# Performance work log

Measured on AMD Instinct MI355X. Metric: run time of the kernel, lower is better.

The kernel has to match this reference:

```python
import jax, jax.numpy as jnp
import numpy as np

FEAT_STRIDE = 16
PRE_NMS_TOP_N = 6000
POST_NMS_TOP_N = 300
NMS_THRESH = 0.7
MIN_SIZE = 16.0
SCALES = np.array([8.0, 16.0, 32.0])
RATIOS = np.array([0.5, 1.0, 2.0])


def _whctrs(a):
    w = a[2] - a[0] + 1.0
    h = a[3] - a[1] + 1.0
    return w, h, a[0] + 0.5 * (w - 1.0), a[1] + 0.5 * (h - 1.0)


def _mkanchors(ws, hs, xc, yc):
    ws = np.asarray(ws).reshape(-1, 1)
    hs = np.asarray(hs).reshape(-1, 1)
    return np.hstack([xc - 0.5 * (ws - 1.0), yc - 0.5 * (hs - 1.0),
                      xc + 0.5 * (ws - 1.0), yc + 0.5 * (hs - 1.0)])


def generate_anchors(base_size, ratios, scales):
    base = np.array([1.0, 1.0, base_size, base_size]) - 1.0
    w, h, xc, yc = _whctrs(base)
    size = w * h
    ws = np.round(np.sqrt(size / ratios))
    hs = np.round(ws * ratios)
    ratio_anchors = _mkanchors(ws, hs, xc, yc)
    out = []
    for i in range(ratio_anchors.shape[0]):
        w, h, xc, yc = _whctrs(ratio_anchors[i])
        out.append(_mkanchors(w * scales, h * scales, xc, yc))
    return np.vstack(out)


def _nms(boxes, scores, thresh, max_out):
    # greedy NMS, boxes [N,4], scores [N] (-inf = invalid). Returns idx [max_out], valid [max_out]
    N = boxes.shape[0]
    x1, y1, x2, y2 = boxes[:, 0], boxes[:, 1], boxes[:, 2], boxes[:, 3]
    areas = (x2 - x1 + 1.0) * (y2 - y1 + 1.0)
    ar = jnp.arange(N)

    def step(s, _):
        i = jnp.argmax(s)
        valid = s[i] > -jnp.inf
        b = boxes[i]
        xx1 = jnp.maximum(b[0], x1)
        yy1 = jnp.maximum(b[1], y1)
        xx2 = jnp.minimum(b[2], x2)
        yy2 = jnp.minimum(b[3], y2)
        inter = jnp.maximum(0.0, xx2 - xx1 + 1.0) * jnp.maximum(0.0, yy2 - yy1 + 1.0)
        iou = inter / (areas[i] + areas - inter)
        sup = (iou > thresh) | (ar == i)
        return jnp.where(sup, -jnp.inf, s), (i, valid)

    _, (idx, valid) = jax.lax.scan(step, scores, None, length=max_out)
    return idx, valid


def setup_inputs() -> dict:
    key = jax.random.key(0)
    k1, k2 = jax.random.split(key)
    B, A, Hf, Wf = 16, 9, 160, 160
    scores_map = jax.random.uniform(k1, (B, 2 * A, Hf, Wf), dtype=jnp.float32)
    bbox_deltas = jax.random.normal(k2, (B, 4 * A, Hf, Wf), dtype=jnp.float32) * 0.2
    im_info = jnp.tile(jnp.array([[Hf * FEAT_STRIDE, Wf * FEAT_STRIDE, 1.0]], jnp.float32), (B, 1))
    return {"scores_map": scores_map, "bbox_deltas": bbox_deltas, "im_info": im_info}


def reference(scores_map, bbox_deltas, im_info):
    anchors0 = jnp.asarray(generate_anchors(16, RATIOS, SCALES), jnp.float32)  # [A,4]
    A = anchors0.shape[0]
    B, _, Hf, Wf = scores_map.shape
    # fg scores: [B, A, H, W] -> [B, H*W*A]
    scores = scores_map[:, A:].transpose(0, 2, 3, 1).reshape(B, -1)
    deltas = bbox_deltas.transpose(0, 2, 3, 1).reshape(B, -1, 4)  # [B, H*W*A, 4]
    sx = (jnp.arange(Wf) * FEAT_STRIDE).astype(jnp.float32)
    sy = (jnp.arange(Hf) * FEAT_STRIDE).astype(jnp.float32)
    SX, SY = jnp.meshgrid(sx, sy)  # [H, W]
    shifts = jnp.stack([SX.ravel(), SY.ravel(), SX.ravel(), SY.ravel()], axis=1)  # [K,4]
    all_anchors = (shifts[:, None, :] + anchors0[None, :, :]).reshape(-1, 4)  # [K*A, 4]

    aw = all_anchors[:, 2] - all_anchors[:, 0] + 1.0
    ah = all_anchors[:, 3] - all_anchors[:, 1] + 1.0
    acx = all_anchors[:, 0] + 0.5 * aw
    acy = all_anchors[:, 1] + 0.5 * ah

    def single(s, d, info):
        # bbox_transform_inv
        pcx = d[:, 0] * aw + acx
        pcy = d[:, 1] * ah + acy
        pw = jnp.exp(d[:, 2]) * aw
        ph = jnp.exp(d[:, 3]) * ah
        x1 = jnp.clip(pcx - 0.5 * pw, 0.0, info[1] - 1.0)
        y1 = jnp.clip(pcy - 0.5 * ph, 0.0, info[0] - 1.0)
        x2 = jnp.clip(pcx + 0.5 * pw, 0.0, info[1] - 1.0)
        y2 = jnp.clip(pcy + 0.5 * ph, 0.0, info[0] - 1.0)
        boxes = jnp.stack([x1, y1, x2, y2], axis=1)
        ms = MIN_SIZE * info[2]
        keep = ((x2 - x1 + 1.0) >= ms) & ((y2 - y1 + 1.0) >= ms)
        s = jnp.where(keep, s, -jnp.inf)
        top_s, top_i = jax.lax.top_k(s, PRE_NMS_TOP_N)
        top_b = boxes[top_i]
        idx, valid = _nms(top_b, top_s, NMS_THRESH, POST_NMS_TOP_N)
        return jnp.where(valid[:, None], top_b[idx], 0.0)  # [POST, 4]

    out_boxes = jax.vmap(single)(scores, deltas, im_info)  # [B, POST, 4]
    batch_col = jnp.broadcast_to(
        jnp.arange(B, dtype=out_boxes.dtype)[:, None, None], (B, POST_NMS_TOP_N, 1))
    return jnp.concatenate([batch_col, out_boxes], axis=2)  # [B, POST, 5]
```

## Files before the change

### kernel.cpp

```cpp
#include <hip/hip_runtime.h>
#include <cstdint>
#include <cstddef>

typedef unsigned int u32;
typedef unsigned long long u64;

#define NBATCH 16
#define NA 9
#define HF 160
#define WF 160
#define HWC (HF*WF)
#define NPB (NA*HWC)
#define PRE_N 6000
#define POST_N 300
#define SEL_CAP 8192
#define NBIN 2048
#define UNI_BINS 2048
#define NMS_W 16

__constant__ float c_AW[9] = {184.f,368.f,736.f,128.f,256.f,512.f,88.f,176.f,352.f};
__constant__ float c_AH[9] = {96.f,192.f,384.f,128.f,256.f,512.f,176.f,352.f,704.f};

__device__ __forceinline__ void box_core(
    float d0, float d1, float d2, float d3, int a, int x, int y,
    float imH, float imW, float ms,
    float& x1, float& y1, float& x2, float& y2, bool& keep)
{
  float aw = c_AW[a], ah = c_AH[a];
  float acx = (float)x * 16.0f + 8.0f;
  float acy = (float)y * 16.0f + 8.0f;
  float pcx = d0 * aw + acx;
  float pcy = d1 * ah + acy;
  float pw  = expf(d2) * aw;
  float ph  = expf(d3) * ah;
  x1 = fminf(fmaxf(pcx - 0.5f * pw, 0.0f), imW - 1.0f);
  y1 = fminf(fmaxf(pcy - 0.5f * ph, 0.0f), imH - 1.0f);
  x2 = fminf(fmaxf(pcx + 0.5f * pw, 0.0f), imW - 1.0f);
  y2 = fminf(fmaxf(pcy + 0.5f * ph, 0.0f), imH - 1.0f);
  keep = ((x2 - x1 + 1.0f) >= ms) && ((y2 - y1 + 1.0f) >= ms);
}

__device__ __forceinline__ void box_from_deltas(
    const float* __restrict__ bd, int b, int a, int pos,
    float imH, float imW, float ms,
    float& x1, float& y1, float& x2, float& y2, bool& keep)
{
  int y = pos / WF;
  int x = pos - y * WF;
  size_t base = ((size_t)(b * 4 * NA) + 4 * a) * HWC + (size_t)pos;
  float d0 = bd[base];
  float d1 = bd[base + HWC];
  float d2 = bd[base + 2 * HWC];
  float d3 = bd[base + 3 * HWC];
  box_core(d0, d1, d2, d3, a, x, y, imH, imW, ms, x1, y1, x2, y2, keep);
}

__device__ __forceinline__ u32 desc_enc(float s) {
  u32 su = __float_as_uint(s);
  u32 asc = (su & 0x80000000u) ? ~su : (su | 0x80000000u);
  return ~asc;
}

__device__ __forceinline__ bool iou_gt(float inter, float uni) {
  float ss = fmaf(0.7f, uni, -inter);
  if (fabsf(ss) <= uni * 1e-6f) return (inter / uni > 0.7f);
  return ss < 0.0f;
}

__global__ void __launch_bounds__(256) k_scores_hist(
    const float* __restrict__ sm, const float* __restrict__ bd,
    const float* __restrict__ info, u32* __restrict__ keys, u32* __restrict__ hist) {
  __shared__ u32 lh[UNI_BINS];
  int img   = blockIdx.x / 45;
  int rem   = blockIdx.x - img * 45;
  int a     = rem / 5;
  int chunk = rem - a * 5;
  int tid = threadIdx.x;
  for (int i = tid; i < UNI_BINS; i += 256) lh[i] = 0;
  __syncthreads();
  float imH = info[img*3+0], imW = info[img*3+1], ms = 16.0f * info[img*3+2];
  const float* sp = sm + ((size_t)(img * 2 * NA) + NA + a) * HWC;
  const float* dp = bd + ((size_t)(img * 4 * NA) + 4 * a) * HWC;
  u32* kp = keys + (size_t)img * NPB + (size_t)a * HWC;
  for (int j = 0; j < 5; j++) {
    int pos0 = (chunk * 1280 + j * 256 + tid) * 4;
    float4 s4  = *(const float4*)&sp[pos0];
    float4 q0  = *(const float4*)&dp[pos0];
    float4 q1  = *(const float4*)&dp[HWC + pos0];
    float4 q2  = *(const float4*)&dp[2*HWC + pos0];
    float4 q3  = *(const float4*)&dp[3*HWC + pos0];
    float sv[4] = {s4.x, s4.y, s4.z, s4.w};
    float v0[4] = {q0.x, q0.y, q0.z, q0.w};
    float v1[4] = {q1.x, q1.y, q1.z, q1.w};
    float v2[4] = {q2.x, q2.y, q2.z, q2.w};
    float v3[4] = {q3.x, q3.y, q3.z, q3.w};
    u32 kq[4];
    #pragma unroll
    for (int e = 0; e < 4; e++) {
      int pos = pos0 + e;
      int y = pos / WF;
      int x = pos - y * WF;
      float x1, y1, x2, y2; bool keep;
      box_core(v0[e], v1[e], v2[e], v3[e], a, x, y, imH, imW, ms, x1, y1, x2, y2, keep);
      float s = sv[e];
      if (!keep) s = __uint_as_float(0xFF800000u);
      kq[e] = desc_enc(s);
      int q = (int)floorf(s * (float)UNI_BINS);
      q = q < 0 ? 0 : (q > UNI_BINS - 1 ? UNI_BINS - 1 : q);
      atomicAdd(&lh[(UNI_BINS - 1) - q], 1u);
    }
    *(uint4*)&kp[pos0] = make_uint4(kq[0], kq[1], kq[2], kq[3]);
  }
  __syncthreads();
  u32* gh = hist + img * UNI_BINS;
  for (int i = tid; i < UNI_BINS; i += 256) { u32 v = lh[i]; if (v) atomicAdd(&gh[i], v); }
}

__global__ void __launch_bounds__(256) k_select(
    const u32* __restrict__ keys, const u32* __restrict__ hist, u64* __restrict__ thresh_arr) {
  int img = blockIdx.x, tid = threadIdx.x;
  __shared__ u32 sc[256];
  __shared__ u32 lh[NBIN];
  __shared__ u64 sh_thresh;
  __shared__ int sh_state;
  __shared__ u64 sh_prefix;
  __shared__ u32 sh_kth;
  const u32* gh = hist + img * UNI_BINS;
  u32 loc[8]; u32 tot = 0;
  for (int j = 0; j < 8; j++) { loc[j] = gh[tid * 8 + j]; tot += loc[j]; }
  if (tid == 0) { sh_state = 0; sh_prefix = 0; sh_kth = PRE_N; }
  sc[tid] = tot;
  __syncthreads();
  for (int off = 1; off < 256; off <<= 1) {
    u32 v = sc[tid]; u32 a = (tid >= off) ? sc[tid - off] : 0u;
    __syncthreads(); sc[tid] = v + a; __syncthreads();
  }
  u32 incl = sc[tid], excl = incl - tot;
  if (PRE_N > excl && PRE_N <= incl) {
    u32 run = excl;
    for (int j = 0; j < 8; j++) {
      run += loc[j];
      if (run >= PRE_N) {
        int b = tid * 8 + j;
        if (b < UNI_BINS - 1 && run <= SEL_CAP) {
          float sb = (float)(UNI_BINS - 1 - b) * (1.0f / (float)UNI_BINS);
          sh_thresh = ((u64)desc_enc(sb) << 32) | 0xFFFFFFFFull;
          sh_state = 1;
        }
        break;
      }
    }
  }
  __syncthreads();
  if (!sh_state) {
    const u32* kp = keys + (size_t)img * NPB;
    const int shifts[6] = {53, 42, 31, 20, 9, 0};
    const int widths[6] = {11, 11, 11, 11, 11, 9};
    for (int p = 0; p < 6; p++) {
      if (sh_state) break;
      for (int i = tid; i < NBIN; i += 256) lh[i] = 0;
      __syncthreads();
      u64 prefix = sh_prefix; u32 kth = sh_kth;
      int shift = shifts[p], width = widths[p];
      u32 nb = 1u << width;
      int hs = shift + width;
      for (int i = tid; i < NPB; i += 256) {
        int a = i / HWC;
        int pos = i - a * HWC;
        u64 key = ((u64)kp[i] << 32) | (u64)(u32)(pos * NA + a);
        bool m = (p == 0) || ((key >> hs) == prefix);
        if (m) atomicAdd(&lh[(u32)(key >> shift) & (nb - 1u)], 1u);
      }
      __syncthreads();
      u32 l2[8]; u32 t2 = 0;
      for (int j = 0; j < 8; j++) {
        u32 b = (u32)(tid * 8 + j);
        u32 v = (b < nb) ? lh[b] : 0u;
        l2[j] = v; t2 += v;
      }
      sc[tid] = t2; __syncthreads();
      for (int off = 1; off < 256; off <<= 1) {
        u32 v = sc[tid]; u32 a = (tid >= off) ? sc[tid - off] : 0u;
        __syncthreads(); sc[tid] = v + a; __syncthreads();
      }
      u32 incl2 = sc[tid], excl2 = incl2 - t2;
      if (kth > excl2 && kth <= incl2) {
        u32 run = excl2;
        for (int j = 0; j < 8; j++) {
          run += l2[j];
          if (run >= kth) {
            u32 bin = (u32)(tid * 8 + j);
            u32 below = run - l2[j];
            u32 cnt = l2[j];
            u32 knew = kth - below;
            u64 pfull = (prefix << width) | (u64)bin;
            u32 M = (u32)PRE_N - knew + cnt;
            if (M <= SEL_CAP) {
              u64 lowmask = (shift > 0) ? ((1ULL << shift) - 1ULL) : 0ULL;
              sh_thresh = (pfull << shift) | lowmask;
              sh_state = 1;
            } else {
              sh_prefix = pfull; sh_kth = knew;
            }
            break;
          }
        }
      }
      __syncthreads();
    }
  }
  if (tid == 0) thresh_arr[img] = sh_thresh;
}

__global__ void __launch_bounds__(256) k_compact(
    const u32* __restrict__ keys, const u64* __restrict__ thresh,
    u32* __restrict__ selcnt, u64* __restrict__ sel,
    const float* __restrict__ bd, const float* __restrict__ info,
    float4* __restrict__ boxsel) {
  int img = blockIdx.y;
  int tid = threadIdx.x;
  u64 T = thresh[img];
  int t0 = blockIdx.x * 3840;
  const u32* kp = keys + (size_t)img * NPB + t0;
  u64 fk[15];
  u32 mycnt = 0;
  #pragma unroll
  for (int j = 0; j < 15; j++) {
    int t = t0 + j * 256 + tid;
    u32 d = kp[j * 256 + tid];
    int a = t / HWC;
    int pos = t - a * HWC;
    u64 key = ((u64)d << 32) | (u64)(u32)(pos * NA + a);
    fk[j] = key;
    if (key <= T) mycnt++;
  }
  __shared__ u32 sc[256];
  __shared__ u32 sbase;
  sc[tid] = mycnt;
  __syncthreads();
  for (int off = 1; off < 256; off <<= 1) {
    u32 v = sc[tid];
    u32 add = (tid >= off) ? sc[tid - off] : 0u;
    __syncthreads();
    sc[tid] = v + add;
    __syncthreads();
  }
  if (tid == 255 && sc[255] > 0) sbase = atomicAdd(&selcnt[img], sc[255]);
  __syncthreads();
  if (mycnt == 0) return;
  u32 myoff = sbase + sc[tid] - mycnt;
  u64* sp = sel + (size_t)img * SEL_CAP;
  float4* bp = boxsel + (size_t)img * SEL_CAP;
  float imH = info[img*3+0], imW = info[img*3+1], ms = 16.0f * info[img*3+2];
  u32 c = 0;
  #pragma unroll
  for (int j = 0; j < 15; j++) {
    u64 key = fk[j];
    if (key <= T) {
      u32 p = myoff + c;
      if (p < SEL_CAP) {
        u32 desc = (u32)(key >> 32);
        u32 idx = (u32)key;
        sp[p] = ((u64)desc << 31) | ((u64)idx << 13) | (u64)p;
        int a = (int)(idx % NA);
        int pos = (int)(idx / NA);
        float x1, y1, x2, y2; bool keep;
        box_from_deltas(bd, img, a, pos, imH, imW, ms, x1, y1, x2, y2, keep);
        bp[p] = make_float4(x1, y1, x2, y2);
      }
      c++;
    }
  }
}

__global__ void __launch_bounds__(256) k_sort1(u64* __restrict__ sel, const u32* __restrict__ selcnt) {
  __shared__ u64 s[1024];
  int img = blockIdx.y, c = blockIdx.x, tid = threadIdx.x;
  u32 cnt = selcnt[img]; if (cnt > SEL_CAP) cnt = SEL_CAP;
  u64* sp = sel + (size_t)img * SEL_CAP + (size_t)c * 1024;
  int gbase = c * 1024;
  for (int i = tid; i < 1024; i += 256) s[i] = ((u32)(gbase + i) < cnt) ? sp[i] : ~0ULL;
  __syncthreads();
  for (int k = 2; k <= 1024; k <<= 1) {
    for (int j = k >> 1; j > 0; j >>= 1) {
      for (int i = tid; i < 1024; i += 256) {
        int p = i ^ j;
        if (p > i) {
          u64 a = s[i], b = s[p];
          bool up = ((i & k) == 0);
          if (up ? (a > b) : (a < b)) { s[i] = b; s[p] = a; }
        }
      }
      __syncthreads();
    }
  }
  for (int i = tid; i < 1024; i += 256) sp[i] = s[i];
}

__global__ void __launch_bounds__(1024) k_sort2(
    const u64* __restrict__ sel, const float4* __restrict__ boxsel,
    float4* __restrict__ boxes, u32* __restrict__ nvalid) {
  __shared__ u64 s[SEL_CAP];
  __shared__ int sh_nv;
  int img = blockIdx.x;
  int tid = threadIdx.x;
  const u64* sp = sel + (size_t)img * SEL_CAP;
  if (tid == 0) sh_nv = PRE_N;
  for (int i = tid; i < SEL_CAP; i += 1024) s[i] = sp[i];
  __syncthreads();
  int d0 = tid * 8;
  for (int L = 1024; L < SEL_CAP; L <<= 1) {
    int pairBase = d0 & ~(2 * L - 1);
    int d = d0 - pairBase;
    const u64* A = s + pairBase;
    const u64* B = s + pairBase + L;
    int lo = d - L; if (lo < 0) lo = 0;
    int hi = (d < L) ? d : L;
    while (lo < hi) {
      int mid = (lo + hi) >> 1;
      if (A[mid] <= B[d - 1 - mid]) lo = mid + 1; else hi = mid;
    }
    int ia = lo, ib = d - lo;
    u64 o[8];
    #pragma unroll
    for (int k = 0; k < 8; k++) {
      bool ta = (ib >= L) || (ia < L && A[ia] <= B[ib]);
      o[k] = ta ? A[ia++] : B[ib++];
    }
    __syncthreads();
    #pragma unroll
    for (int k = 0; k < 8; k++) s[d0 + k] = o[k];
    __syncthreads();
  }
  const float4* bp = boxsel + (size_t)img * SEL_CAP;
  for (int r = tid; r < PRE_N; r += 1024) {
    u64 key = s[r];
    u32 desc = (u32)(key >> 31);
    bool valid = desc < 0xFF800000u;
    if (!valid) atomicMin(&sh_nv, r);
    float4 bx = valid ? bp[key & 0x1FFFu] : make_float4(0.f, 0.f, 0.f, 0.f);
    boxes[(size_t)img * PRE_N + r] = bx;
  }
  __syncthreads();
  if (tid == 0) nvalid[img] = (u32)sh_nv;
}

__global__ void __launch_bounds__(NMS_W*64) k_nms(const float4* __restrict__ boxes,
                                                  const u32* __restrict__ nvalid_arr,
                                                  float* __restrict__ out) {
  __shared__ float4 kbox[POST_N];
  __shared__ float karea[POST_N];
  __shared__ u64 kcodeW[(POST_N + 7) / 8];
  __shared__ float4 cb[2][64];
  __shared__ float car[2][64];
  __shared__ int cint[2][64];
  __shared__ u64 wcol[2][64];
  __shared__ u64 supw[2][NMS_W];
  __shared__ int sh_nkept;
  int img = blockIdx.x;
  int tid = threadIdx.x;
  int lane = tid & 63;
  int wv = tid >> 6;
  int nvalid = (int)nvalid_arr[img];
  if (nvalid > PRE_N) nvalid = PRE_N;
  const float4* bb = boxes + (size_t)img * PRE_N;
  if (tid == 0) sh_nkept = 0;
  if (tid < 64) {
    float4 c = (tid < nvalid) ? bb[tid] : make_float4(0.f, 0.f, 0.f, 0.f);
    cb[0][tid] = c;
    float A = (c.z - c.x + 1.0f) * (c.w - c.y + 1.0f);
    car[0][tid] = A;
    cint[0][tid] = (int)rintf(8.0f * log2f(A));
  } else if (tid < 128) {
    wcol[0][tid - 64] = 0;
  } else if (tid < 128 + NMS_W) {
    supw[0][tid - 128] = 0;
  }
  __syncthreads();
  int pb = 0;
  for (int base = 0; base < nvalid; base += 64, pb ^= 1) {
    int nk = sh_nkept;
    if (nk >= POST_N) break;
    int bn = nvalid - base; if (bn > 64) bn = 64;
    bool sup;
    u64 colpart = 0;
    {
      bool inb = lane < bn;
      sup = !inb;
      if (inb) {
        float4 C = cb[pb][lane];
        float A0 = car[pb][lane];
        int myc = cint[pb][lane];
        int nw = (nk + 7) >> 3;
        for (int jw = wv; jw < nw; jw += NMS_W) {
          u64 w = kcodeW[jw];
          int jbase = jw << 3;
          int jm = nk - jbase; if (jm > 8) jm = 8;
          for (int k = 0; k < jm; k++) {
            int d = (int)((w >> (k * 8)) & 0xFFu) - myc;
            if (d > 5 || d < -5) continue;
            int j = jbase + k;
            float4 K = kbox[j];
            float xx1 = fmaxf(K.x, C.x);
            float yy1 = fmaxf(K.y, C.y);
            float xx2 = fminf(K.z, C.z);
            float yy2 = fminf(K.w, C.w);
            float iw = fmaxf(0.0f, xx2 - xx1 + 1.0f);
            float ih = fmaxf(0.0f, yy2 - yy1 + 1.0f);
            float inter = iw * ih;
            float uni = (karea[j] + A0) - inter;
            sup = sup | iou_gt(inter, uni);
          }
        }
        for (int i = wv; i < lane; i += NMS_W) {
          if (i >= bn) break;
          float Ai = car[pb][i];
          if (Ai <= 0.6999f * A0 || A0 <= 0.6999f * Ai) continue;
          float4 I4 = cb[pb][i];
          float xx1 = fmaxf(I4.x, C.x);
          float yy1 = fmaxf(I4.y, C.y);
          float xx2 = fminf(I4.z, C.z);
          float yy2 = fminf(I4.w, C.w);
          float iw = fmaxf(0.0f, xx2 - xx1 + 1.0f);
          float ih = fmaxf(0.0f, yy2 - yy1 + 1.0f);
          float inter = iw * ih;
          float uni = (Ai + A0) - inter;
          if (iou_gt(inter, uni)) colpart |= 1ULL << i;
        }
      }
    }
    u64 bm = __ballot(sup);
    if (lane == 0) supw[pb][wv] = bm;
    if (colpart) atomicOr(&wcol[pb][lane], colpart);
    __syncthreads();
    if (wv == 0) {
      u64 so = (lane < NMS_W) ? supw[pb][lane] : 0ULL;
      so |= __shfl_xor(so, 1);
      so |= __shfl_xor(so, 2);
      so |= __shfl_xor(so, 4);
      so |= __shfl_xor(so, 8);
      so = __shfl(so, 0);
      u64 validm = (bn >= 64) ? ~0ULL : ((1ULL << bn) - 1ULL);
      u64 colm = wcol[pb][lane];
      u64 live = validm & ~so;
      u64 km = 0;
      int cnt = nk;
      while (live && cnt < POST_N) {
        int c = __ffsll((long long)live) - 1;
        km |= 1ULL << c;
        cnt++;
        u64 dead = __ballot((colm >> c) & 1ULL);
        live &= ~dead;
        live &= ~(1ULL << c);
      }
      if ((km >> lane) & 1ULL) {
        int rank = nk + (int)__popcll(km & ((1ULL << lane) - 1ULL));
        float4 C = cb[pb][lane];
        kbox[rank] = C;
        karea[rank] = car[pb][lane];
        ((unsigned char*)kcodeW)[rank] = (unsigned char)cint[pb][lane];
        float* o = out + ((size_t)img * POST_N + rank) * 5;
        o[0] = (float)img; o[1] = C.x; o[2] = C.y; o[3] = C.z; o[4] = C.w;
      }
      if (lane == 0) sh_nkept = cnt;
    } else if (wv == 1) {
      int nb2 = base + 64;
      if (nb2 < nvalid) {
        int i = nb2 + lane;
        float4 c = (i < nvalid) ? bb[i] : make_float4(0.f, 0.f, 0.f, 0.f);
        cb[pb ^ 1][lane] = c;
        float A = (c.z - c.x + 1.0f) * (c.w - c.y + 1.0f);
        car[pb ^ 1][lane] = A;
        cint[pb ^ 1][lane] = (int)rintf(8.0f * log2f(A));
      }
    } else if (wv == 2) {
      wcol[pb ^ 1][lane] = 0;
      if (lane < NMS_W) supw[pb ^ 1][lane] = 0;
    }
    __syncthreads();
  }
  int fk = sh_nkept;
  for (int r = fk + tid; r < POST_N; r += NMS_W*64) {
    float* o = out + ((size_t)img * POST_N + r) * 5;
    o[0] = (float)img; o[1] = 0.f; o[2] = 0.f; o[3] = 0.f; o[4] = 0.f;
  }
}

extern "C" void kernel_launch(void* const* d_in, const int* in_sizes, int n_in,
                              void* d_out, int out_size, void* d_ws, size_t ws_size,
                              hipStream_t stream) {
  const float* sm   = (const float*)d_in[0];
  const float* bd   = (const float*)d_in[1];
  const float* info = (const float*)d_in[2];
  float* out = (float*)d_out;
  char* ws = (char*)d_ws;

  size_t off = 0;
  auto alloc = [&](size_t bytes) { size_t o = off; off += (bytes + 255) & ~(size_t)255; return o; };
  u32* keys     = (u32*)(ws + alloc((size_t)NBATCH * NPB * 4));
  size_t off_hist = alloc((size_t)NBATCH * UNI_BINS * 4);
  u32* hist     = (u32*)(ws + off_hist);
  u32* selcnt   = (u32*)(ws + alloc(NBATCH * 4));
  size_t zero_end = off;
  u64* thresh   = (u64*)(ws + alloc(NBATCH * 8));
  u32* nvalid   = (u32*)(ws + alloc(NBATCH * 4));
  u64* sel      = (u64*)(ws + alloc((size_t)NBATCH * SEL_CAP * 8));
  float4* boxsel= (float4*)(ws + alloc((size_t)NBATCH * SEL_CAP * 16));
  float4* boxes = (float4*)(ws + alloc((size_t)NBATCH * PRE_N * 16));
  (void)ws_size; (void)in_sizes; (void)n_in; (void)out_size;

  hipMemsetAsync(ws + off_hist, 0, zero_end - off_hist, stream);
  hipLaunchKernelGGL(k_scores_hist, dim3(720), dim3(256), 0, stream, sm, bd, info, keys, hist);
  hipLaunchKernelGGL(k_select, dim3(16), dim3(256), 0, stream, keys, hist, thresh);
  hipLaunchKernelGGL(k_compact, dim3(60, 16), dim3(256), 0, stream, keys, thresh, selcnt, sel, bd, info, boxsel);
  hipLaunchKernelGGL(k_sort1, dim3(8, 16), dim3(256), 0, stream, sel, selcnt);
  hipLaunchKernelGGL(k_sort2, dim3(16), dim3(1024), 0, stream, sel, boxsel, boxes, nvalid);
  hipLaunchKernelGGL(k_nms, dim3(16), dim3(NMS_W*64), 0, stream, boxes, nvalid, out);
}
```

Before: 231.6 us.

## Fuse merge sort with NMS and shrink bitonic chunk to 512

Merges the final merge-sort kernel and the NMS kernel into one block per image. The sorted keys are turned into 16-bit slot indices in a shared-memory union, and boxes are gathered straight from boxsel during NMS. This removes a kernel launch and the global round trip of the sorted box array and nvalid. The bitonic pre-sort chunk is also halved, doubling its block count, which adds one extra merge level in the fused kernel.

```diff
diff --git a/kernel.cpp b/kernel.cpp
--- a/kernel.cpp
+++ b/kernel.cpp
@@ -3,6 +3,7 @@
 #include <cstddef>
 
 typedef unsigned int u32;
+typedef unsigned short u16;
 typedef unsigned long long u64;
 
 #define NBATCH 16
@@ -17,6 +18,7 @@
 #define NBIN 2048
 #define UNI_BINS 2048
 #define NMS_W 16
+#define CHUNK 512
 
 __constant__ float c_AW[9] = {184.f,368.f,736.f,128.f,256.f,512.f,88.f,176.f,352.f};
 __constant__ float c_AH[9] = {96.f,192.f,384.f,128.f,256.f,512.f,176.f,352.f,704.f};
@@ -274,16 +276,16 @@
 }
 
 __global__ void __launch_bounds__(256) k_sort1(u64* __restrict__ sel, const u32* __restrict__ selcnt) {
-  __shared__ u64 s[1024];
+  __shared__ u64 s[CHUNK];
   int img = blockIdx.y, c = blockIdx.x, tid = threadIdx.x;
   u32 cnt = selcnt[img]; if (cnt > SEL_CAP) cnt = SEL_CAP;
-  u64* sp = sel + (size_t)img * SEL_CAP + (size_t)c * 1024;
-  int gbase = c * 1024;
-  for (int i = tid; i < 1024; i += 256) s[i] = ((u32)(gbase + i) < cnt) ? sp[i] : ~0ULL;
-  __syncthreads();
-  for (int k = 2; k <= 1024; k <<= 1) {
+  u64* sp = sel + (size_t)img * SEL_CAP + (size_t)c * CHUNK;
+  int gbase = c * CHUNK;
+  for (int i = tid; i < CHUNK; i += 256) s[i] = ((u32)(gbase + i) < cnt) ? sp[i] : ~0ULL;
+  __syncthreads();
+  for (int k = 2; k <= CHUNK; k <<= 1) {
     for (int j = k >> 1; j > 0; j >>= 1) {
-      for (int i = tid; i < 1024; i += 256) {
+      for (int i = tid; i < CHUNK; i += 256) {
         int p = i ^ j;
         if (p > i) {
           u64 a = s[i], b = s[p];
@@ -294,26 +296,41 @@
       __syncthreads();
     }
   }
-  for (int i = tid; i < 1024; i += 256) sp[i] = s[i];
-}
-
-__global__ void __launch_bounds__(1024) k_sort2(
-    const u64* __restrict__ sel, const float4* __restrict__ boxsel,
-    float4* __restrict__ boxes, u32* __restrict__ nvalid) {
-  __shared__ u64 s[SEL_CAP];
+  for (int i = tid; i < CHUNK; i += 256) sp[i] = s[i];
+}
+
+__global__ void __launch_bounds__(1024) k_sort2nms(
+    const u64* __restrict__ sel, const u32* __restrict__ selcnt,
+    const float4* __restrict__ boxsel, float* __restrict__ out) {
+  union SB {
+    u64 s[SEL_CAP];
+    struct {
+      u16 slot16[PRE_N + 64];
+      float4 kbox[POST_N];
+      float karea[POST_N];
+      u64 kcodeW[(POST_N + 7) / 8];
+      float4 cb[2][64];
+      float car[2][64];
+      int cint[2][64];
+      u64 wcol[2][64];
+      u64 supw[2][NMS_W];
+    } n;
+  };
+  __shared__ SB u;
   __shared__ int sh_nv;
+  __shared__ int sh_nkept;
   int img = blockIdx.x;
   int tid = threadIdx.x;
   const u64* sp = sel + (size_t)img * SEL_CAP;
-  if (tid == 0) sh_nv = PRE_N;
-  for (int i = tid; i < SEL_CAP; i += 1024) s[i] = sp[i];
+  if (tid == 0) { sh_nv = PRE_N; sh_nkept = 0; }
+  for (int i = tid; i < SEL_CAP; i += 1024) u.s[i] = sp[i];
   __syncthreads();
   int d0 = tid * 8;
-  for (int L = 1024; L < SEL_CAP; L <<= 1) {
+  for (int L = CHUNK; L < SEL_CAP; L <<= 1) {
     int pairBase = d0 & ~(2 * L - 1);
     int d = d0 - pairBase;
-    const u64* A = s + pairBase;
-    const u64* B = s + pairBase + L;
+    const u64* A = u.s + pairBase;
+    const u64* B = u.s + pairBase + L;
     int lo = d - L; if (lo < 0) lo = 0;
     int hi = (d < L) ? d : L;
     while (lo < hi) {
@@ -329,52 +346,40 @@
     }
     __syncthreads();
     #pragma unroll
-    for (int k = 0; k < 8; k++) s[d0 + k] = o[k];
-    __syncthreads();
-  }
-  const float4* bp = boxsel + (size_t)img * SEL_CAP;
-  for (int r = tid; r < PRE_N; r += 1024) {
-    u64 key = s[r];
-    u32 desc = (u32)(key >> 31);
-    bool valid = desc < 0xFF800000u;
-    if (!valid) atomicMin(&sh_nv, r);
-    float4 bx = valid ? bp[key & 0x1FFFu] : make_float4(0.f, 0.f, 0.f, 0.f);
-    boxes[(size_t)img * PRE_N + r] = bx;
-  }
-  __syncthreads();
-  if (tid == 0) nvalid[img] = (u32)sh_nv;
-}
-
-__global__ void __launch_bounds__(NMS_W*64) k_nms(const float4* __restrict__ boxes,
-                                                  const u32* __restrict__ nvalid_arr,
-                                                  float* __restrict__ out) {
-  __shared__ float4 kbox[POST_N];
-  __shared__ float karea[POST_N];
-  __shared__ u64 kcodeW[(POST_N + 7) / 8];
-  __shared__ float4 cb[2][64];
-  __shared__ float car[2][64];
-  __shared__ int cint[2][64];
-  __shared__ u64 wcol[2][64];
-  __shared__ u64 supw[2][NMS_W];
-  __shared__ int sh_nkept;
-  int img = blockIdx.x;
-  int tid = threadIdx.x;
+    for (int k = 0; k < 8; k++) u.s[d0 + k] = o[k];
+    __syncthreads();
+  }
+  u64 rv[6];
+  {
+    int k = 0;
+    for (int r = tid; r < PRE_N; r += 1024, k++) rv[k] = u.s[r];
+    __syncthreads();
+    k = 0;
+    for (int r = tid; r < PRE_N; r += 1024, k++) {
+      u64 key = rv[k];
+      u32 desc = (u32)(key >> 31);
+      bool valid = desc < 0xFF800000u;
+      if (!valid) atomicMin(&sh_nv, r);
+      u.n.slot16[r] = valid ? (u16)(key & 0x1FFFu) : (u16)0xFFFF;
+    }
+  }
+  __syncthreads();
   int lane = tid & 63;
   int wv = tid >> 6;
-  int nvalid = (int)nvalid_arr[img];
+  int nvalid = sh_nv;
   if (nvalid > PRE_N) nvalid = PRE_N;
-  const float4* bb = boxes + (size_t)img * PRE_N;
-  if (tid == 0) sh_nkept = 0;
+  const float4* bp = boxsel + (size_t)img * SEL_CAP;
   if (tid < 64) {
-    float4 c = (tid < nvalid) ? bb[tid] : make_float4(0.f, 0.f, 0.f, 0.f);
-    cb[0][tid] = c;
+    float4 c = make_float4(0.f, 0.f, 0.f, 0.f);
+    if (tid < nvalid) { u16 sl = u.n.slot16[tid]; c = bp[sl]; }
+    u.n.cb[0][tid] = c;
     float A = (c.z - c.x + 1.0f) * (c.w - c.y + 1.0f);
-    car[0][tid] = A;
-    cint[0][tid] = (int)rintf(8.0f * log2f(A));
+    u.n.car[0][tid] = A;
+    u.n.cint[0][tid] = (int)rintf(8.0f * log2f(A));
   } else if (tid < 128) {
-    wcol[0][tid - 64] = 0;
+    u.n.wcol[0][tid - 64] = 0;
   } else if (tid < 128 + NMS_W) {
-    supw[0][tid - 128] = 0;
+    u.n.supw[0][tid - 128] = 0;
   }
   __syncthreads();
   int pb = 0;
@@ -388,19 +393,19 @@
       bool inb = lane < bn;
       sup = !inb;
       if (inb) {
-        float4 C = cb[pb][lane];
-        float A0 = car[pb][lane];
-        int myc = cint[pb][lane];
+        float4 C = u.n.cb[pb][lane];
+        float A0 = u.n.car[pb][lane];
+        int myc = u.n.cint[pb][lane];
         int nw = (nk + 7) >> 3;
         for (int jw = wv; jw < nw; jw += NMS_W) {
-          u64 w = kcodeW[jw];
+          u64 w = u.n.kcodeW[jw];
           int jbase = jw << 3;
           int jm = nk - jbase; if (jm > 8) jm = 8;
           for (int k = 0; k < jm; k++) {
             int d = (int)((w >> (k * 8)) & 0xFFu) - myc;
             if (d > 5 || d < -5) continue;
             int j = jbase + k;
-            float4 K = kbox[j];
+            float4 K = u.n.kbox[j];
             float xx1 = fmaxf(K.x, C.x);
             float yy1 = fmaxf(K.y, C.y);
             float xx2 = fminf(K.z, C.z);
@@ -408,15 +413,15 @@
             float iw = fmaxf(0.0f, xx2 - xx1 + 1.0f);
             float ih = fmaxf(0.0f, yy2 - yy1 + 1.0f);
             float inter = iw * ih;
-            float uni = (karea[j] + A0) - inter;
+            float uni = (u.n.karea[j] + A0) - inter;
             sup = sup | iou_gt(inter, uni);
           }
         }
         for (int i = wv; i < lane; i += NMS_W) {
           if (i >= bn) break;
-          float Ai = car[pb][i];
+          float Ai = u.n.car[pb][i];
           if (Ai <= 0.6999f * A0 || A0 <= 0.6999f * Ai) continue;
-          float4 I4 = cb[pb][i];
+          float4 I4 = u.n.cb[pb][i];
           float xx1 = fmaxf(I4.x, C.x);
           float yy1 = fmaxf(I4.y, C.y);
           float xx2 = fminf(I4.z, C.z);
@@ -430,18 +435,18 @@
       }
     }
     u64 bm = __ballot(sup);
-    if (lane == 0) supw[pb][wv] = bm;
-    if (colpart) atomicOr(&wcol[pb][lane], colpart);
+    if (lane == 0) u.n.supw[pb][wv] = bm;
+    if (colpart) atomicOr(&u.n.wcol[pb][lane], colpart);
     __syncthreads();
     if (wv == 0) {
-      u64 so = (lane < NMS_W) ? supw[pb][lane] : 0ULL;
+      u64 so = (lane < NMS_W) ? u.n.supw[pb][lane] : 0ULL;
       so |= __shfl_xor(so, 1);
       so |= __shfl_xor(so, 2);
       so |= __shfl_xor(so, 4);
       so |= __shfl_xor(so, 8);
       so = __shfl(so, 0);
       u64 validm = (bn >= 64) ? ~0ULL : ((1ULL << bn) - 1ULL);
-      u64 colm = wcol[pb][lane];
+      u64 colm = u.n.wcol[pb][lane];
       u64 live = validm & ~so;
       u64 km = 0;
       int cnt = nk;
@@ -455,10 +460,10 @@
       }
       if ((km >> lane) & 1ULL) {
         int rank = nk + (int)__popcll(km & ((1ULL << lane) - 1ULL));
-        float4 C = cb[pb][lane];
-        kbox[rank] = C;
-        karea[rank] = car[pb][lane];
-        ((unsigned char*)kcodeW)[rank] = (unsigned char)cint[pb][lane];
+        float4 C = u.n.cb[pb][lane];
+        u.n.kbox[rank] = C;
+        u.n.karea[rank] = u.n.car[pb][lane];
+        ((unsigned char*)u.n.kcodeW)[rank] = (unsigned char)u.n.cint[pb][lane];
         float* o = out + ((size_t)img * POST_N + rank) * 5;
         o[0] = (float)img; o[1] = C.x; o[2] = C.y; o[3] = C.z; o[4] = C.w;
       }
@@ -467,20 +472,21 @@
       int nb2 = base + 64;
       if (nb2 < nvalid) {
         int i = nb2 + lane;
-        float4 c = (i < nvalid) ? bb[i] : make_float4(0.f, 0.f, 0.f, 0.f);
-        cb[pb ^ 1][lane] = c;
+        float4 c = make_float4(0.f, 0.f, 0.f, 0.f);
+        if (i < nvalid) { u16 sl = u.n.slot16[i]; c = bp[sl]; }
+        u.n.cb[pb ^ 1][lane] = c;
         float A = (c.z - c.x + 1.0f) * (c.w - c.y + 1.0f);
-        car[pb ^ 1][lane] = A;
-        cint[pb ^ 1][lane] = (int)rintf(8.0f * log2f(A));
+        u.n.car[pb ^ 1][lane] = A;
+        u.n.cint[pb ^ 1][lane] = (int)rintf(8.0f * log2f(A));
       }
     } else if (wv == 2) {
-      wcol[pb ^ 1][lane] = 0;
-      if (lane < NMS_W) supw[pb ^ 1][lane] = 0;
+      u.n.wcol[pb ^ 1][lane] = 0;
+      if (lane < NMS_W) u.n.supw[pb ^ 1][lane] = 0;
     }
     __syncthreads();
   }
   int fk = sh_nkept;
-  for (int r = fk + tid; r < POST_N; r += NMS_W*64) {
+  for (int r = fk + tid; r < POST_N; r += NMS_W * 64) {
     float* o = out + ((size_t)img * POST_N + r) * 5;
     o[0] = (float)img; o[1] = 0.f; o[2] = 0.f; o[3] = 0.f; o[4] = 0.f;
   }
@@ -503,17 +509,14 @@
   u32* selcnt   = (u32*)(ws + alloc(NBATCH * 4));
   size_t zero_end = off;
   u64* thresh   = (u64*)(ws + alloc(NBATCH * 8));
-  u32* nvalid   = (u32*)(ws + alloc(NBATCH * 4));
   u64* sel      = (u64*)(ws + alloc((size_t)NBATCH * SEL_CAP * 8));
   float4* boxsel= (float4*)(ws + alloc((size_t)NBATCH * SEL_CAP * 16));
-  float4* boxes = (float4*)(ws + alloc((size_t)NBATCH * PRE_N * 16));
   (void)ws_size; (void)in_sizes; (void)n_in; (void)out_size;
 
   hipMemsetAsync(ws + off_hist, 0, zero_end - off_hist, stream);
   hipLaunchKernelGGL(k_scores_hist, dim3(720), dim3(256), 0, stream, sm, bd, info, keys, hist);
   hipLaunchKernelGGL(k_select, dim3(16), dim3(256), 0, stream, keys, hist, thresh);
   hipLaunchKernelGGL(k_compact, dim3(60, 16), dim3(256), 0, stream, keys, thresh, selcnt, sel, bd, info, boxsel);
-  hipLaunchKernelGGL(k_sort1, dim3(8, 16), dim3(256), 0, stream, sel, selcnt);
-  hipLaunchKernelGGL(k_sort2, dim3(16), dim3(1024), 0, stream, sel, boxsel, boxes, nvalid);
-  hipLaunchKernelGGL(k_nms, dim3(16), dim3(NMS_W*64), 0, stream, boxes, nvalid, out);
-}
+  hipLaunchKernelGGL(k_sort1, dim3(SEL_CAP / CHUNK, 16), dim3(256), 0, stream, sel, selcnt);
+  hipLaunchKernelGGL(k_sort2nms, dim3(16), dim3(1024), 0, stream, sel, selcnt, boxsel, out);
+}
```

After: 211.7 us. -8.6%, faster.
